# Optimization experiments

Hardware: AMD Instinct MI355X
Metric: run time of the kernel (lower is better)

Reference implementation:

```python
import jax, jax.numpy as jnp
import numpy as np
from jax import lax

NG, NF, NW = 5, 10, 8
STEP = NG + NF + 1
MARGIN, LAM, ALPHA, P_W, R_W = 1.0, 0.01, 1.0, 0.7, 0.1
KNUM, KMUL = 5, 2.0
GAMMA = 5.0
BIG = 1e10  # finite stand-in for inf border of the soft-DTW DP (grad-safe)
T, DFEAT = 512, 64


def setup_inputs() -> dict:
    key = jax.random.key(0)
    k1, k2 = jax.random.split(key)
    data = jax.random.normal(k1, (NW * STEP, T, DFEAT), jnp.float32)
    lens = jax.random.randint(k2, (NW * STEP,), T // 2, T + 1, dtype=jnp.int32)
    return {"data": data, "lens": lens}


def _softdtw_R(D):
    # D: [P, N, M] squared-euclidean cost. Returns rows [N, P, M] with
    # rows[i-1, p, j-1] == R[i, j] of the soft-DTW DP recurrence
    # R[i,j] = D[i,j] + softmin_gamma(R[i-1,j], R[i,j-1], R[i-1,j-1]).
    Pn, N, M = D.shape
    row0 = jnp.concatenate([jnp.zeros((Pn, 1), D.dtype), jnp.full((Pn, M), BIG, D.dtype)], axis=1)

    def row_step(prev, d_row):
        up, diag = prev[:, 1:], prev[:, :-1]

        def col_step(left, ins):
            d, u, dg = ins  # each [P]
            smin = -GAMMA * jax.nn.logsumexp(jnp.stack([-left, -u, -dg]) / GAMMA, axis=0)
            r = d + smin
            return r, r

        _, cols = lax.scan(col_step, jnp.full((Pn,), BIG, D.dtype), (d_row.T, up.T, diag.T))
        new_row = jnp.concatenate([jnp.full((Pn, 1), BIG, D.dtype), cols.T], axis=1)
        return new_row, cols.T

    _, rows = lax.scan(row_step, row0, jnp.swapaxes(D, 0, 1))
    return rows


def _mmd(source, target):
    # Standard multi-kernel Gaussian MMD applied to 3-D inputs exactly as the
    # torch code does: L2 distance sums over the time axis only -> [n, n, d].
    ns = source.shape[0]
    total = jnp.concatenate([source, target], axis=0)  # [n, T, d]
    n = total.shape[0]
    sq = jnp.sum(total * total, axis=1)  # [n, d]
    cross = jnp.einsum('atf,btf->abf', total, total)  # [n, n, d]
    L2 = sq[:, None, :] + sq[None, :, :] - 2.0 * cross
    bw = jnp.sum(L2) / (n * n - n)
    bw = bw / (KMUL ** (KNUM // 2))
    K = sum(jnp.exp(-L2 / (bw * KMUL ** i)) for i in range(KNUM))
    XX, YY = K[:ns, :ns], K[ns:, ns:]
    XY, YX = K[:ns, ns:], K[ns:, :ns]
    return jnp.mean(XX + YY - XY - YX)


def _forward(data, lens):
    # Batch all (anchor, positive/negative) pairs across writers.
    anchor_idx = jnp.repeat(jnp.arange(NW) * STEP, NG + NF)                       # [P]
    other_idx = (jnp.arange(NW)[:, None] * STEP + 1 + jnp.arange(NG + NF)[None, :]).ravel()
    X, Y = data[anchor_idx], data[other_idx]  # [P, T, d]
    lx, ly = lens[anchor_idx], lens[other_idx]
    # Pairwise squared distances D[p,i,j] = ||X[p,i] - Y[p,j]||^2
    D = (jnp.sum(X * X, -1)[:, :, None] + jnp.sum(Y * Y, -1)[:, None, :]
         - 2.0 * jnp.einsum('pid,pjd->pij', X, Y))
    rows = _softdtw_R(D)  # [T, P, T]
    Pn = X.shape[0]
    # R[len_a, len_p] only depends on D[:len_a, :len_p], so gathering at the
    # lengths equals running soft-DTW on the length-sliced sequences.
    dist = rows[lx - 1, jnp.arange(Pn), ly - 1] / (lx + ly).astype(data.dtype)
    dist = dist.reshape(NW, NG + NF)
    dg, dn = dist[:, :NG], dist[:, NG:]          # genuine / forgery distances
    only_pos = jnp.sum(dg, axis=1) * (LAM / NG)  # [NW]
    lk1 = jax.nn.relu(dg[:, :, None] + MARGIN - dn[:, None, :5]) * P_W
    lk2 = jax.nn.relu(dg[:, :, None] + MARGIN - dn[:, None, 5:]) * (1.0 - P_W)
    nz = jnp.sum(lk1 != 0, axis=(1, 2)) + jnp.sum(lk2 != 0, axis=(1, 2))  # stop-grad count
    lv = (jnp.sum(lk1, (1, 2)) + jnp.sum(lk2, (1, 2))) / (nz + 1).astype(data.dtype)
    total_loss = jnp.mean(lv + only_pos)
    mmd1 = _mmd(data[0:STEP - 5], data[STEP:2 * STEP - 5]) * ALPHA
    var_g = jnp.var(dg.ravel(), ddof=1) * R_W   # torch.var is unbiased
    return total_loss + mmd1 + var_g


def reference(data, lens):
    return _forward(data, lens)
```

## Files before the change

kernel.cpp:

```cpp
#include <hip/hip_runtime.h>
#include <hip/hip_bf16.h>
#include <cstdint>
#include <cstddef>

#define T_ 512
#define DF 64
#define NPAIR 120
#define STEPW 16
#define NEGS (-(1 << 26))
#define NSK 640

#define C1_ 0.28853900817779268f
#define C2D 3.4657359027997265

__device__ __forceinline__ float wred_sum(float v) {
#pragma unroll
  for (int o = 32; o > 0; o >>= 1) v += __shfl_down(v, o);
  return v;
}

__device__ __forceinline__ int dexp(double x) {
  return (int)((__double_as_longlong(x) >> 52) & 0x7ff) - 1023;
}

#define GLOAD(DST, PTR)                                                    \
  asm volatile("global_load_dwordx4 %0, %1, off"                           \
               : "=&v"(DST) : "v"(PTR) : "memory")

__global__ __launch_bounds__(256) void gemm_mmd_kernel(
    const float* __restrict__ data, float* __restrict__ wbuf, int pair0,
    int npc, float* __restrict__ l2buf, float* __restrict__ bwpart) {
  if ((int)blockIdx.y == npc) {
    const int tid = threadIdx.x;
    const int g = tid >> 6;
    const int f = tid & 63;
    const int b = (int)blockIdx.x * 4 + g;
    if (b < 253) {
      int u = 0, rem = b;
      while (rem >= 22 - u) { rem -= 22 - u; ++u; }
      int v = u + rem;
      float s = 0.f;
      if (u != v) {
        int iu = u < 11 ? u : u + 5;
        int iv = v < 11 ? v : v + 5;
        const float* A = data + (size_t)iu * (T_ * DF) + f;
        const float* B = data + (size_t)iv * (T_ * DF) + f;
#pragma unroll 8
        for (int t = 0; t < T_; ++t) {
          float dd = A[(size_t)t * DF] - B[(size_t)t * DF];
          s = fmaf(dd, dd, s);
        }
      }
      l2buf[(size_t)(u * 22 + v) * 64 + f] = s;
      l2buf[(size_t)(v * 22 + u) * 64 + f] = s;
      float tot = wred_sum(s);
      if (f == 0) bwpart[b] = 2.f * tot;
    }
    return;
  }

  __shared__ float XsT[64][68];
  __shared__ float YsT[64][68];
  __shared__ float nrmx[64];
  __shared__ float nrmy[64];

  const int tile = blockIdx.x;
  const int pc = blockIdx.y;
  const int p = pair0 + pc;
  const int w = p / 15;
  const int o = p - w * 15;
  const int aidx = w * STEPW;
  const int oidx = aidx + 1 + o;
  const int i0 = (tile >> 3) << 6;
  const int j0 = (tile & 7) << 6;
  const int tid = threadIdx.x;

  const float* Xg = data + (size_t)aidx * (T_ * DF);
  const float* Yg = data + (size_t)oidx * (T_ * DF);

#pragma unroll
  for (int l = 0; l < 4; ++l) {
    int idx = tid + l * 256;
    int r = idx >> 4;
    int c = idx & 15;
    float4 xv = reinterpret_cast<const float4*>(Xg + (size_t)(i0 + r) * DF)[c];
    float4 yv = reinterpret_cast<const float4*>(Yg + (size_t)(j0 + r) * DF)[c];
    XsT[4 * c + 0][r] = xv.x; XsT[4 * c + 1][r] = xv.y;
    XsT[4 * c + 2][r] = xv.z; XsT[4 * c + 3][r] = xv.w;
    YsT[4 * c + 0][r] = yv.x; YsT[4 * c + 1][r] = yv.y;
    YsT[4 * c + 2][r] = yv.z; YsT[4 * c + 3][r] = yv.w;
  }
  __syncthreads();

  if (tid < 128) {
    int r = tid & 63;
    float s = 0.f;
    if (tid < 64) {
#pragma unroll
      for (int k = 0; k < 64; ++k) s = fmaf(XsT[k][r], XsT[k][r], s);
      nrmx[r] = s;
    } else {
#pragma unroll
      for (int k = 0; k < 64; ++k) s = fmaf(YsT[k][r], YsT[k][r], s);
      nrmy[r] = s;
    }
  }
  __syncthreads();

  const int tx = tid & 15;
  const int ty = tid >> 4;
  float acc[4][4];
#pragma unroll
  for (int a = 0; a < 4; ++a)
#pragma unroll
    for (int b = 0; b < 4; ++b) acc[a][b] = 0.f;

#pragma unroll 4
  for (int k = 0; k < 64; ++k) {
    float4 xr = *reinterpret_cast<const float4*>(&XsT[k][ty * 4]);
    float4 yr = *reinterpret_cast<const float4*>(&YsT[k][tx * 4]);
    const float xa[4] = {xr.x, xr.y, xr.z, xr.w};
    const float yb[4] = {yr.x, yr.y, yr.z, yr.w};
#pragma unroll
    for (int a = 0; a < 4; ++a)
#pragma unroll
      for (int b = 0; b < 4; ++b) acc[a][b] = fmaf(xa[a], yb[b], acc[a][b]);
  }

  const int g8 = (j0 >> 3) + (tx >> 1);
  const int off = ((tx & 1) << 8) + 4 * g8;
  float* Wp = wbuf + (size_t)pc * (NSK * T_) + off;
#pragma unroll
  for (int a = 0; a < 4; ++a) {
    int ii = ty * 4 + a;
    float nx = nrmx[ii];
    float4 v;
    v.x = __builtin_exp2f(-(nx + nrmy[tx * 4 + 0] - 2.f * acc[a][0]) * C1_);
    v.y = __builtin_exp2f(-(nx + nrmy[tx * 4 + 1] - 2.f * acc[a][1]) * C1_);
    v.z = __builtin_exp2f(-(nx + nrmy[tx * 4 + 2] - 2.f * acc[a][2]) * C1_);
    v.w = __builtin_exp2f(-(nx + nrmy[tx * 4 + 3] - 2.f * acc[a][3]) * C1_);
    *reinterpret_cast<float4*>(Wp + (size_t)(i0 + ii + 2 * g8) * T_) = v;
  }
}

__global__ __launch_bounds__(64) void dtw_mmdk_kernel(
    const float* __restrict__ Wm, const int* __restrict__ lens,
    float* __restrict__ dist, int pair0, int npc,
    const float* __restrict__ l2buf, const float* __restrict__ bwpart,
    float* __restrict__ mmdpart) {
  if ((int)blockIdx.x >= npc) {
    int b = (int)blockIdx.x - npc;
    if (b < 121) {
      int a = b / 11, c = b - a * 11;
      int f = threadIdx.x;
      float bs = 0.f;
      for (int k2 = f; k2 < 253; k2 += 64) bs += bwpart[k2];
      bs = wred_sum(bs);
      float bw = __shfl(bs, 0) * (1.f / (462.f * 4.f));
      float xx = l2buf[(size_t)(a * 22 + c) * 64 + f];
      float yy = l2buf[(size_t)((11 + a) * 22 + (11 + c)) * 64 + f];
      float xy = l2buf[(size_t)(a * 22 + (11 + c)) * 64 + f];
      float yx = l2buf[(size_t)((11 + a) * 22 + c) * 64 + f];
      float term = 0.f;
      float ib = 1.f / bw;
#pragma unroll
      for (int i = 0; i < 5; ++i) {
        term += expf(-xx * ib) + expf(-yy * ib) - expf(-xy * ib)
              - expf(-yx * ib);
        ib *= 0.5f;
      }
      float tt = wred_sum(term);
      if (f == 0) mmdpart[b] = tt;
    }
    return;
  }

  const int pc = blockIdx.x;
  const int p = pair0 + pc;
  const int w = p / 15;
  const int o = p - w * 15;
  const int lx = lens[w * STEPW];
  const int ly = lens[w * STEPW + 1 + o];
  const int l = threadIdx.x;
  const int imax = lx - 1;
  const int jt = ly - 1;
  const int lt = jt >> 3, ct = jt & 7;
  const int M = lt + (imax >> 1);
  const float invl = 1.f / (float)(lx + ly);

  const float* wp = Wm + (size_t)pc * (NSK * T_) + 4 * l;

  float4 K0a, K0b, K1a, K1b, K2a, K2b, K3a, K3b;
  float4 K4a, K4b, K5a, K5b, K6a, K6b, K7a, K7b;
  float4 K8a, K8b, K9a, K9b, K10a, K10b, K11a, K11b;

#define LDROW(A, B, R)                                     \
  {                                                        \
    int r_ = (R); r_ = r_ > 637 ? 637 : r_;                \
    const float* p_ = wp + (size_t)r_ * T_;                \
    GLOAD(A, p_); GLOAD(B, p_ + 256);                      \
  }

  LDROW(K0a, K0b, 0); LDROW(K1a, K1b, 1);
  LDROW(K2a, K2b, 2); LDROW(K3a, K3b, 3);
  LDROW(K4a, K4b, 4); LDROW(K5a, K5b, 5);

  double e0 = 0., e1 = 0., e2 = 0., e3 = 0.;
  double e4 = 0., e5 = 0., e6 = 0., e7 = 0.;
  double e7A = 0.;
  int S = NEGS;
  double pvB = 0.;  int psB = NEGS;

#define SUP(MM, SA0, SA1, SB0, SB1, RA0, RA1, RB0, RB1)                    \
  {                                                                        \
    const int m_ = (MM);                                                   \
    double nvA = __shfl_up(e7A, 1);                                        \
    double nvB = __shfl_up(e7, 1);                                         \
    int ns = __shfl_up(S, 1);                                              \
    LDROW(RA0, RA1, 2 * m_ + 6);                                           \
    LDROW(RB0, RB1, 2 * m_ + 7);                                           \
    asm volatile("s_waitcnt vmcnt(12)" ::: "memory");                      \
    __builtin_amdgcn_sched_barrier(0);                                     \
    const int i = 2 * (m_ - l);                                            \
    double lA = nvA, dA = pvB, lB = nvB, dB2 = nvA;                        \
    int slA = ns, sdA = psB, slB = ns, sdB = ns;                           \
    if (l == 0) {                                                          \
      lA = 0.; slA = NEGS;                                                 \
      dA = (i == 0) ? 1. : 0.; sdA = (i == 0) ? 0 : NEGS;                  \
      lB = 0.; slB = NEGS;                                                 \
      dB2 = 0.; sdB = NEGS;                                                \
    }                                                                      \
    if ((unsigned)i <= (unsigned)imax) {                                   \
      double sum = ((e0 + e1) + (e2 + e3)) + ((e4 + e5) + (e6 + e7));      \
      int NA = max(S + dexp(sum), max(slA + dexp(lA), sdA + dexp(dA)));    \
      const int dS = S - NA;                                               \
      if (dS != 0) {                                                       \
        e0 = ldexp(e0, dS); e1 = ldexp(e1, dS);                            \
        e2 = ldexp(e2, dS); e3 = ldexp(e3, dS);                            \
        e4 = ldexp(e4, dS); e5 = ldexp(e5, dS);                            \
        e6 = ldexp(e6, dS); e7 = ldexp(e7, dS);                            \
      }                                                                    \
      double L = ldexp(lA, slA - NA);                                      \
      double G = ldexp(dA, sdA - NA);                                      \
      const double WA0 = (double)SA0.x, WA1 = (double)SA0.y;               \
      const double WA2 = (double)SA0.z, WA3 = (double)SA0.w;               \
      const double WA4 = (double)SA1.x, WA5 = (double)SA1.y;               \
      const double WA6 = (double)SA1.z, WA7 = (double)SA1.w;               \
      double qa0 = WA0 * ((L + G) + e0);                                   \
      double qa1 = WA1 * (e1 + e0);                                        \
      double qa2 = WA2 * (e2 + e1);                                        \
      double qa3 = WA3 * (e3 + e2);                                        \
      double qa4 = WA4 * (e4 + e3);                                        \
      double qa5 = WA5 * (e5 + e4);                                        \
      double qa6 = WA6 * (e6 + e5);                                        \
      double qa7 = WA7 * (e7 + e6);                                        \
      double a0 = qa0;                                                     \
      double a1 = fma(WA1, a0, qa1);                                       \
      double a2 = fma(WA2, a1, qa2);                                       \
      double a3 = fma(WA3, a2, qa3);                                       \
      double a4 = fma(WA4, a3, qa4);                                       \
      double a5 = fma(WA5, a4, qa5);                                       \
      double a6 = fma(WA6, a5, qa6);                                       \
      double a7 = fma(WA7, a6, qa7);                                       \
      if (i + 1 <= imax) {                                                 \
        int NB = max(NA, max(slB + dexp(lB), sdB + dexp(dB2)));            \
        const int dB = NA - NB;                                            \
        if (dB != 0) {                                                     \
          a0 = ldexp(a0, dB); a1 = ldexp(a1, dB);                          \
          a2 = ldexp(a2, dB); a3 = ldexp(a3, dB);                          \
          a4 = ldexp(a4, dB); a5 = ldexp(a5, dB);                          \
          a6 = ldexp(a6, dB); a7 = ldexp(a7, dB);                          \
        }                                                                  \
        double LB = ldexp(lB, slB - NB);                                   \
        double GB = ldexp(dB2, sdB - NB);                                  \
        const double WB0 = (double)SB0.x, WB1 = (double)SB0.y;             \
        const double WB2 = (double)SB0.z, WB3 = (double)SB0.w;             \
        const double WB4 = (double)SB1.x, WB5 = (double)SB1.y;             \
        const double WB6 = (double)SB1.z, WB7 = (double)SB1.w;             \
        double qb0 = WB0 * ((LB + GB) + a0);                               \
        double qb1 = WB1 * (a1 + a0);                                      \
        double qb2 = WB2 * (a2 + a1);                                      \
        double qb3 = WB3 * (a3 + a2);                                      \
        double qb4 = WB4 * (a4 + a3);                                      \
        double qb5 = WB5 * (a5 + a4);                                      \
        double qb6 = WB6 * (a6 + a5);                                      \
        double qb7 = WB7 * (a7 + a6);                                      \
        e0 = qb0;                                                          \
        e1 = fma(WB1, e0, qb1);                                            \
        e2 = fma(WB2, e1, qb2);                                            \
        e3 = fma(WB3, e2, qb3);                                            \
        e4 = fma(WB4, e3, qb4);                                            \
        e5 = fma(WB5, e4, qb5);                                            \
        e6 = fma(WB6, e5, qb6);                                            \
        e7 = fma(WB7, e6, qb7);                                            \
        e7A = a7;                               \
        S = NB;                                                            \
      } else {                                                             \
        e0 = a0; e1 = a1; e2 = a2; e3 = a3;                                \
        e4 = a4; e5 = a5; e6 = a6; e7 = a7;                                \
        e7A = a7;                                                          \
        S = NA;                                                            \
      }                                                                    \
    }                                                                      \
    pvB = nvB; psB = ns;                                                   \
  }

  const int nsup = (M + 6) / 6 * 6;
  for (int mb = 0; mb < nsup; mb += 6) {
    SUP(mb + 0, K0a, K0b, K1a, K1b, K6a, K6b, K7a, K7b);
    SUP(mb + 1, K2a, K2b, K3a, K3b, K8a, K8b, K9a, K9b);
    SUP(mb + 2, K4a, K4b, K5a, K5b, K10a, K10b, K11a, K11b);
    SUP(mb + 3, K6a, K6b, K7a, K7b, K0a, K0b, K1a, K1b);
    SUP(mb + 4, K8a, K8b, K9a, K9b, K2a, K2b, K3a, K3b);
    SUP(mb + 5, K10a, K10b, K11a, K11b, K4a, K4b, K5a, K5b);
  }

  asm volatile("s_waitcnt vmcnt(0)" ::: "memory");

  if (l == lt) {
    double out_v = (ct == 0) ? e0 : (ct == 1) ? e1 : (ct == 2) ? e2
                 : (ct == 3) ? e3 : (ct == 4) ? e4 : (ct == 5) ? e5
                 : (ct == 6) ? e6 : e7;
    double vv = (out_v > 0.) ? out_v : 1e-300;
    double r = -C2D * (log2(vv) + (double)S);
    dist[p] = (float)(r * (double)invl);
  }
}

__global__ __launch_bounds__(64) void finalize_kernel(
    const float* __restrict__ dist, const float* __restrict__ mmdpart,
    float* __restrict__ out) {
  int lane = threadIdx.x;
  float lv_po = 0.f;
  float dg[5];
#pragma unroll
  for (int g = 0; g < 5; ++g) dg[g] = 0.f;
  if (lane < 8) {
    const float* dr = dist + lane * 15;
    float dn[10];
#pragma unroll
    for (int g = 0; g < 5; ++g) dg[g] = dr[g];
#pragma unroll
    for (int k = 0; k < 10; ++k) dn[k] = dr[5 + k];
    float s1 = 0.f, s2 = 0.f;
    int nz = 0;
#pragma unroll
    for (int g = 0; g < 5; ++g) {
#pragma unroll
      for (int k = 0; k < 5; ++k) {
        float v2 = dg[g] + 1.0f - dn[k];
        if (v2 > 0.f) { s1 += v2; ++nz; }
      }
#pragma unroll
      for (int k = 5; k < 10; ++k) {
        float v2 = dg[g] + 1.0f - dn[k];
        if (v2 > 0.f) { s2 += v2; ++nz; }
      }
    }
    float only_pos = (dg[0] + dg[1] + dg[2] + dg[3] + dg[4]) * 0.002f;
    float lv = (s1 * 0.7f + s2 * 0.3f) / (float)(nz + 1);
    lv_po = lv + only_pos;
  }
  float tl = wred_sum(lv_po);
  tl = __shfl(tl, 0);

  float psum = dg[0] + dg[1] + dg[2] + dg[3] + dg[4];
  float tsum = wred_sum(psum);
  float mean = __shfl(tsum, 0) * (1.f / 40.f);
  float pdev = 0.f;
  if (lane < 8) {
#pragma unroll
    for (int g = 0; g < 5; ++g) {
      float dd = dg[g] - mean;
      pdev = fmaf(dd, dd, pdev);
    }
  }
  float tdev = wred_sum(pdev);
  tdev = __shfl(tdev, 0);

  float msum = 0.f;
  for (int k2 = lane; k2 < 121; k2 += 64) msum += mmdpart[k2];
  float mt = wred_sum(msum);

  if (lane == 0) {
    float total_loss = tl * (1.f / 8.f);
    float var_g = (tdev / 39.f) * 0.1f;
    float mmd = mt * (1.f / 7744.f);
    out[0] = total_loss + mmd + var_g;
  }
}

__global__ __launch_bounds__(64) void zero_out_kernel(float* __restrict__ out,
                                                      int n) {
  int i = blockIdx.x * 64 + threadIdx.x;
  if (i < n) out[i] = 0.f;
}

extern "C" void kernel_launch(void* const* d_in, const int* in_sizes, int n_in,
                              void* d_out, int out_size, void* d_ws,
                              size_t ws_size, hipStream_t stream) {
  const float* data = (const float*)d_in[0];
  const int* lens = (const int*)d_in[1];
  float* out = (float*)d_out;
  char* ws = (char*)d_ws;

  const size_t HDR = 131072;
  const size_t per_pair = (size_t)NSK * T_ * sizeof(float);

  if (ws_size < HDR + per_pair) {
    zero_out_kernel<<<dim3((out_size + 63) / 64), 64, 0, stream>>>(out,
                                                                   out_size);
    return;
  }

  float* dist = (float*)(ws + 0);
  float* bwpart = (float*)(ws + 1024);
  float* mmdpart = (float*)(ws + 3072);
  float* l2buf = (float*)(ws + 4096);
  float* wbuf = (float*)(ws + HDR);

  size_t avail = ws_size - HDR;
  int PC = (int)(avail / per_pair);
  if (PC > NPAIR) PC = NPAIR;

  for (int p0 = 0; p0 < NPAIR; p0 += PC) {
    int pc = (NPAIR - p0) < PC ? (NPAIR - p0) : PC;
    int first = (p0 == 0) ? 1 : 0;
    gemm_mmd_kernel<<<dim3(64, pc + first), 256, 0, stream>>>(
        data, wbuf, p0, pc, l2buf, bwpart);
    dtw_mmdk_kernel<<<dim3(pc + (first ? 121 : 0)), 64, 0, stream>>>(
        wbuf, lens, dist, p0, pc, l2buf, bwpart, mmdpart);
  }
  finalize_kernel<<<dim3(1), 64, 0, stream>>>(dist, mmdpart, out);
}
```

Measured before the change: 208.2 us.

## Compute pairwise distance GEMM with split-bf16 MFMA instead of FP32 FMA

Replaces the scalar FP32 outer-product loop for the X·Y^T cost tile with MFMA 16x16x32 bf16 instructions. Each input is split into high and low bf16 parts, and three cross products (hh, hl, lh) approximate FP32 accuracy. Shared memory is re-laid out as XOR-swizzled bf16 arrays to avoid bank conflicts. Writes to the weight buffer become scalar stores instead of float4 stores. The split-bf16 scheme loses some precision relative to FP32, and the exponentiated costs feed a long soft-DTW recurrence.

After: 181.3 us. 12.9% less time.

```diff
diff --git a/kernel.cpp b/kernel.cpp
--- a/kernel.cpp
+++ b/kernel.cpp
@@ -13,6 +13,10 @@
 #define C1_ 0.28853900817779268f
 #define C2D 3.4657359027997265
 
+typedef unsigned short ushort_t;
+using f32x4 = __attribute__((ext_vector_type(4))) float;
+using bf16x8 = __attribute__((ext_vector_type(8))) short;
+
 __device__ __forceinline__ float wred_sum(float v) {
 #pragma unroll
   for (int o = 32; o > 0; o >>= 1) v += __shfl_down(v, o);
@@ -21,6 +25,15 @@
 
 __device__ __forceinline__ int dexp(double x) {
   return (int)((__double_as_longlong(x) >> 52) & 0x7ff) - 1023;
+}
+
+__device__ __forceinline__ ushort_t f2bf(float x) {
+  __hip_bfloat16 h = __float2bfloat16(x);
+  return *reinterpret_cast<ushort_t*>(&h);
+}
+__device__ __forceinline__ float bf2f(ushort_t u) {
+  __hip_bfloat16 h = *reinterpret_cast<__hip_bfloat16*>(&u);
+  return __bfloat162float(h);
 }
 
 #define GLOAD(DST, PTR)                                                    \
@@ -30,6 +43,10 @@
 __global__ __launch_bounds__(256) void gemm_mmd_kernel(
     const float* __restrict__ data, float* __restrict__ wbuf, int pair0,
     int npc, float* __restrict__ l2buf, float* __restrict__ bwpart) {
+  __shared__ ushort_t XH[4096], XL[4096], YH[4096], YL[4096];
+  __shared__ float nrmx[64];
+  __shared__ float nrmy[64];
+
   if ((int)blockIdx.y == npc) {
     const int tid = threadIdx.x;
     const int g = tid >> 6;
@@ -59,11 +76,6 @@
     return;
   }
 
-  __shared__ float XsT[64][68];
-  __shared__ float YsT[64][68];
-  __shared__ float nrmx[64];
-  __shared__ float nrmy[64];
-
   const int tile = blockIdx.x;
   const int pc = blockIdx.y;
   const int p = pair0 + pc;
@@ -83,12 +95,21 @@
     int idx = tid + l * 256;
     int r = idx >> 4;
     int c = idx & 15;
+    int g = c >> 1, h = c & 1;
+    int base = r * 64 + ((g ^ (r & 7)) << 3) + (h << 2);
     float4 xv = reinterpret_cast<const float4*>(Xg + (size_t)(i0 + r) * DF)[c];
     float4 yv = reinterpret_cast<const float4*>(Yg + (size_t)(j0 + r) * DF)[c];
-    XsT[4 * c + 0][r] = xv.x; XsT[4 * c + 1][r] = xv.y;
-    XsT[4 * c + 2][r] = xv.z; XsT[4 * c + 3][r] = xv.w;
-    YsT[4 * c + 0][r] = yv.x; YsT[4 * c + 1][r] = yv.y;
-    YsT[4 * c + 2][r] = yv.z; YsT[4 * c + 3][r] = yv.w;
+    const float xa[4] = {xv.x, xv.y, xv.z, xv.w};
+    const float ya[4] = {yv.x, yv.y, yv.z, yv.w};
+#pragma unroll
+    for (int e = 0; e < 4; ++e) {
+      ushort_t xh = f2bf(xa[e]);
+      XH[base + e] = xh;
+      XL[base + e] = f2bf(xa[e] - bf2f(xh));
+      ushort_t yh = f2bf(ya[e]);
+      YH[base + e] = yh;
+      YL[base + e] = f2bf(ya[e] - bf2f(yh));
+    }
   }
   __syncthreads();
 
@@ -97,49 +118,69 @@
     float s = 0.f;
     if (tid < 64) {
 #pragma unroll
-      for (int k = 0; k < 64; ++k) s = fmaf(XsT[k][r], XsT[k][r], s);
+      for (int k = 0; k < 64; ++k) {
+        int a = r * 64 + (((k >> 3) ^ (r & 7)) << 3) + (k & 7);
+        float x = bf2f(XH[a]) + bf2f(XL[a]);
+        s = fmaf(x, x, s);
+      }
       nrmx[r] = s;
     } else {
 #pragma unroll
-      for (int k = 0; k < 64; ++k) s = fmaf(YsT[k][r], YsT[k][r], s);
+      for (int k = 0; k < 64; ++k) {
+        int a = r * 64 + (((k >> 3) ^ (r & 7)) << 3) + (k & 7);
+        float y = bf2f(YH[a]) + bf2f(YL[a]);
+        s = fmaf(y, y, s);
+      }
       nrmy[r] = s;
     }
   }
   __syncthreads();
 
-  const int tx = tid & 15;
-  const int ty = tid >> 4;
-  float acc[4][4];
-#pragma unroll
-  for (int a = 0; a < 4; ++a)
-#pragma unroll
-    for (int b = 0; b < 4; ++b) acc[a][b] = 0.f;
-
-#pragma unroll 4
-  for (int k = 0; k < 64; ++k) {
-    float4 xr = *reinterpret_cast<const float4*>(&XsT[k][ty * 4]);
-    float4 yr = *reinterpret_cast<const float4*>(&YsT[k][tx * 4]);
-    const float xa[4] = {xr.x, xr.y, xr.z, xr.w};
-    const float yb[4] = {yr.x, yr.y, yr.z, yr.w};
-#pragma unroll
-    for (int a = 0; a < 4; ++a)
-#pragma unroll
-      for (int b = 0; b < 4; ++b) acc[a][b] = fmaf(xa[a], yb[b], acc[a][b]);
-  }
-
-  const int g8 = (j0 >> 3) + (tx >> 1);
-  const int off = ((tx & 1) << 8) + 4 * g8;
-  float* Wp = wbuf + (size_t)pc * (NSK * T_) + off;
-#pragma unroll
-  for (int a = 0; a < 4; ++a) {
-    int ii = ty * 4 + a;
-    float nx = nrmx[ii];
-    float4 v;
-    v.x = __builtin_exp2f(-(nx + nrmy[tx * 4 + 0] - 2.f * acc[a][0]) * C1_);
-    v.y = __builtin_exp2f(-(nx + nrmy[tx * 4 + 1] - 2.f * acc[a][1]) * C1_);
-    v.z = __builtin_exp2f(-(nx + nrmy[tx * 4 + 2] - 2.f * acc[a][2]) * C1_);
-    v.w = __builtin_exp2f(-(nx + nrmy[tx * 4 + 3] - 2.f * acc[a][3]) * C1_);
-    *reinterpret_cast<float4*>(Wp + (size_t)(i0 + ii + 2 * g8) * T_) = v;
+  const int lane = tid & 63;
+  const int wid = tid >> 6;
+  const int rowA = 16 * wid + (lane & 15);
+  const int b16 = lane >> 4;
+
+  const int aA0 = rowA * 64 + (((b16) ^ (rowA & 7)) << 3);
+  const int aA1 = rowA * 64 + (((4 + b16) ^ (rowA & 7)) << 3);
+  bf16x8 ah0 = *reinterpret_cast<const bf16x8*>(&XH[aA0]);
+  bf16x8 ah1 = *reinterpret_cast<const bf16x8*>(&XH[aA1]);
+  bf16x8 al0 = *reinterpret_cast<const bf16x8*>(&XL[aA0]);
+  bf16x8 al1 = *reinterpret_cast<const bf16x8*>(&XL[aA1]);
+
+  float* WpBase = wbuf + (size_t)pc * (NSK * T_);
+  const float nx[4] = {nrmx[16 * wid + 0 + 4 * b16], 0.f, 0.f, 0.f};
+  (void)nx;
+
+#pragma unroll
+  for (int t = 0; t < 4; ++t) {
+    const int rowB = 16 * t + (lane & 15);
+    const int aB0 = rowB * 64 + (((b16) ^ (rowB & 7)) << 3);
+    const int aB1 = rowB * 64 + (((4 + b16) ^ (rowB & 7)) << 3);
+    bf16x8 bh0 = *reinterpret_cast<const bf16x8*>(&YH[aB0]);
+    bf16x8 bh1 = *reinterpret_cast<const bf16x8*>(&YH[aB1]);
+    bf16x8 bl0 = *reinterpret_cast<const bf16x8*>(&YL[aB0]);
+    bf16x8 bl1 = *reinterpret_cast<const bf16x8*>(&YL[aB1]);
+
+    f32x4 acc = {0.f, 0.f, 0.f, 0.f};
+    acc = __builtin_amdgcn_mfma_f32_16x16x32_bf16(ah0, bh0, acc, 0, 0, 0);
+    acc = __builtin_amdgcn_mfma_f32_16x16x32_bf16(ah1, bh1, acc, 0, 0, 0);
+    acc = __builtin_amdgcn_mfma_f32_16x16x32_bf16(ah0, bl0, acc, 0, 0, 0);
+    acc = __builtin_amdgcn_mfma_f32_16x16x32_bf16(ah1, bl1, acc, 0, 0, 0);
+    acc = __builtin_amdgcn_mfma_f32_16x16x32_bf16(al0, bh0, acc, 0, 0, 0);
+    acc = __builtin_amdgcn_mfma_f32_16x16x32_bf16(al1, bh1, acc, 0, 0, 0);
+
+    const int jg = j0 + 16 * t + (lane & 15);
+    const float ny = nrmy[16 * t + (lane & 15)];
+    const int g8 = jg >> 3;
+    const int off = (((jg >> 2) & 1) << 8) + 4 * g8 + (jg & 3);
+#pragma unroll
+    for (int r = 0; r < 4; ++r) {
+      const int ig = i0 + 16 * wid + 4 * b16 + r;
+      float d = nrmx[16 * wid + 4 * b16 + r] + ny - 2.f * acc[r];
+      float wv = __builtin_exp2f(-d * C1_);
+      WpBase[(size_t)(ig + 2 * g8) * T_ + off] = wv;
+    }
   }
 }
 
@@ -293,7 +334,7 @@
         e5 = fma(WB5, e4, qb5);                                            \
         e6 = fma(WB6, e5, qb6);                                            \
         e7 = fma(WB7, e6, qb7);                                            \
-        e7A = a7;                               \
+        e7A = a7;                                                          \
         S = NB;                                                            \
       } else {                                                             \
         e0 = a0; e1 = a1; e2 = a2; e3 = a3;                                \
```
